# Kernel optimization log

Measured on AMD Instinct MI355X. Metric: run time of the kernel, lower is better.

Reference implementation:

```python
import jax, jax.numpy as jnp
import numpy as np
from jax import lax

WIN = 7
K1 = 0.01
K2 = 0.03


def _box(t, w):
    # 'valid' box filter: uniform WINxWIN window, matches F.conv2d(t, w)
    return lax.conv_general_dilated(
        t, w, window_strides=(1, 1), padding='VALID',
        dimension_numbers=('NCHW', 'OIHW', 'NCHW'))


def setup_inputs() -> dict:
    key = jax.random.key(0)
    kx, ky = jax.random.split(key)
    X = jax.random.uniform(kx, (256, 1, 320, 320), dtype=jnp.float32)
    Y = jax.random.uniform(ky, (256, 1, 320, 320), dtype=jnp.float32)
    return {"X": X, "Y": Y}


def reference(X, Y):
    NP = WIN * WIN
    cov_norm = NP / (NP - 1)  # unbiased covariance correction
    w = jnp.ones((1, 1, WIN, WIN), X.dtype) / NP

    # per-sample dynamic range of the reference image Y -> [B,1,1,1]
    data_range = jnp.max(Y, axis=(1, 2, 3), keepdims=True)
    C1 = (K1 * data_range) ** 2
    C2 = (K2 * data_range) ** 2

    ux = _box(X, w)
    uy = _box(Y, w)
    uxx = _box(X * X, w)
    uyy = _box(Y * Y, w)
    uxy = _box(X * Y, w)

    vx = cov_norm * (uxx - ux * ux)
    vy = cov_norm * (uyy - uy * uy)
    vxy = cov_norm * (uxy - ux * uy)

    A1 = 2 * ux * uy + C1
    A2 = 2 * vxy + C2
    B1 = ux * ux + uy * uy + C1
    B2 = vx + vy + C2

    S = (A1 * A2) / (B1 * B2)
    S = jnp.mean(S)          # reduced=True
    return 1.0 - S           # as_loss=True
```

## Files before the change

kernel.cpp:

```cpp
#include <hip/hip_runtime.h>

#define BATCH 256
#define IMH 320
#define IMW 320
#define OUTD 314
#define NCH 9
#define NSTRIP 3
#define RCH 36
#define ITERS 42

__global__ __launch_bounds__(256) void k_max(const float* __restrict__ Y,
                                             unsigned* __restrict__ dr) {
    int bid = blockIdx.x;
    int b = bid >> 2, part = bid & 3;
    const float4* p = (const float4*)(Y + (size_t)b * (IMH * IMW) + part * (IMH * IMW / 4));
    float m = 0.f;
    for (int i = threadIdx.x; i < (IMH * IMW / 16); i += 256) {
        float4 v = p[i];
        m = fmaxf(m, fmaxf(fmaxf(v.x, v.y), fmaxf(v.z, v.w)));
    }
    for (int off = 32; off; off >>= 1) m = fmaxf(m, __shfl_down(m, off, 64));
    __shared__ float sm[4];
    int lane = threadIdx.x & 63, wv = threadIdx.x >> 6;
    if (lane == 0) sm[wv] = m;
    __syncthreads();
    if (threadIdx.x == 0) {
        m = fmaxf(fmaxf(sm[0], sm[1]), fmaxf(sm[2], sm[3]));
        atomicMax(dr + b, __float_as_uint(m));
    }
}

__device__ __forceinline__ float ssim_px(float hx, float hy, float hp, float hxy,
                                         float C1, float C2) {
    const float inv = 1.f / 49.f;
    const float cn  = 49.f / 48.f;
    float ux  = hx  * inv, uy = hy * inv;
    float upp = hp  * inv;
    float uxy = hxy * inv;
    float ux2 = ux * ux, uy2 = uy * uy, uxuy = ux * uy;
    float B2 = cn * (upp - ux2 - uy2) + C2;
    float A2 = 2.f * cn * (uxy - uxuy) + C2;
    float A1 = 2.f * uxuy + C1;
    float B1 = ux2 + uy2 + C1;
    return (A1 * A2) * __builtin_amdgcn_rcpf(B1 * B2);
}

__device__ __forceinline__ float bperm(int addr, float v) {
    return __int_as_float(__builtin_amdgcn_ds_bpermute(addr, __float_as_int(v)));
}

template<bool FULL>
__device__ __forceinline__ float strip_loop(const float2* __restrict__ Xp,
                                            const float2* __restrict__ Yp,
                                            int r0, int nout,
                                            int a1, int a2, int a3,
                                            bool valid, float C1, float C2) {
    float2 rx[7], ry[7];
    #pragma unroll
    for (int k = 0; k < 7; ++k) { rx[k] = make_float2(0.f, 0.f); ry[k] = make_float2(0.f, 0.f); }
    float2 sx  = make_float2(0.f, 0.f), sy  = make_float2(0.f, 0.f);
    float2 sp  = make_float2(0.f, 0.f), sxy = make_float2(0.f, 0.f);
    float part = 0.f;

    #define HQ(q, h0, h1) {                                                    \
        float s2_ = q.x + q.y;                                                 \
        float b1_ = bperm(a1, s2_);                                            \
        float b2_ = bperm(a2, s2_);                                            \
        float b3_ = bperm(a3, s2_);                                            \
        float y3_ = bperm(a3, q.y);                                            \
        float S8_ = (s2_ + b1_) + (b2_ + b3_);                                 \
        h0 = S8_ - y3_;  h1 = S8_ - q.x; }

    #define VBODY(K, I7) {                                                     \
        const int i = (I7) + (K);                                              \
        const int r = r0 + i;                                                  \
        float2 xn = make_float2(0.f, 0.f), yn = make_float2(0.f, 0.f);         \
        if (FULL || r < IMH) { xn = Xp[r * (IMW/2)]; yn = Yp[r * (IMW/2)]; }   \
        const float2 ox = rx[K], oy = ry[K];                                   \
        sx.x  += xn.x - ox.x;              sx.y  += xn.y - ox.y;               \
        sy.x  += yn.x - oy.x;              sy.y  += yn.y - oy.y;               \
        sp.x  += (xn.x*xn.x + yn.x*yn.x) - (ox.x*ox.x + oy.x*oy.x);            \
        sp.y  += (xn.y*xn.y + yn.y*yn.y) - (ox.y*ox.y + oy.y*oy.y);            \
        sxy.x += xn.x*yn.x - ox.x*oy.x;    sxy.y += xn.y*yn.y - ox.y*oy.y;     \
        rx[K] = xn; ry[K] = yn;                                                \
        if (i >= 6 && (FULL || (i - 6) < nout)) {                              \
            float hx0,hx1,hy0,hy1,hp0,hp1,hq0,hq1;                             \
            HQ(sx,  hx0, hx1)                                                  \
            HQ(sy,  hy0, hy1)                                                  \
            HQ(sp,  hp0, hp1)                                                  \
            HQ(sxy, hq0, hq1)                                                  \
            float s0 = ssim_px(hx0, hy0, hp0, hq0, C1, C2);                    \
            float s1 = ssim_px(hx1, hy1, hp1, hq1, C1, C2);                    \
            part += valid ? (s0 + s1) : 0.f;                                   \
        }                                                                      \
    }

    for (int i7 = 0; i7 < ITERS; i7 += 7) {
        VBODY(0, i7) VBODY(1, i7) VBODY(2, i7) VBODY(3, i7)
        VBODY(4, i7) VBODY(5, i7) VBODY(6, i7)
    }
    #undef VBODY
    #undef HQ
    return part;
}

__global__ __launch_bounds__(64) void k_ssim(const float* __restrict__ X,
                                             const float* __restrict__ Y,
                                             const unsigned* __restrict__ dr,
                                             double* __restrict__ acc) {
    const int idx = blockIdx.x;
    const int b   = idx / (NCH * NSTRIP);
    const int rem = idx - b * (NCH * NSTRIP);
    const int rc  = rem / NSTRIP;
    const int s   = rem - rc * NSTRIP;
    const int l   = threadIdx.x;
    const int r0  = rc * RCH;
    const int nout = min(RCH, OUTD - r0);

    const int in_base = (s == 0) ? 0 : (s == 1 ? 122 : 192);
    const int lane_lo = (s == 2) ? 26 : 0;
    const bool valid  = (l >= lane_lo) && (l <= 60);

    const float2* Xp = (const float2*)(X + (size_t)b * (IMH * IMW)) + (in_base >> 1) + l;
    const float2* Yp = (const float2*)(Y + (size_t)b * (IMH * IMW)) + (in_base >> 1) + l;

    const int a1 = ((l + 1) & 63) << 2;
    const int a2 = ((l + 2) & 63) << 2;
    const int a3 = ((l + 3) & 63) << 2;

    const float drv = __uint_as_float(dr[b]);
    const float c1s = 0.01f * drv, c2s = 0.03f * drv;
    const float C1 = c1s * c1s, C2 = c2s * c2s;

    float part;
    if (r0 + ITERS <= IMH) {
        part = strip_loop<true >(Xp, Yp, r0, nout, a1, a2, a3, valid, C1, C2);
    } else {
        part = strip_loop<false>(Xp, Yp, r0, nout, a1, a2, a3, valid, C1, C2);
    }

    for (int off = 32; off; off >>= 1) part += __shfl_down(part, off, 64);
    if (l == 0) atomicAdd(acc, (double)part);
}

__global__ void k_final(const double* __restrict__ acc, float* __restrict__ out) {
    const double cnt = (double)BATCH * (double)OUTD * (double)OUTD;
    out[0] = (float)(1.0 - acc[0] / cnt);
}

extern "C" void kernel_launch(void* const* d_in, const int* in_sizes, int n_in,
                              void* d_out, int out_size, void* d_ws, size_t ws_size,
                              hipStream_t stream) {
    const float* X = (const float*)d_in[0];
    const float* Y = (const float*)d_in[1];
    float* out = (float*)d_out;

    unsigned* dr = (unsigned*)d_ws;
    double* acc  = (double*)((char*)d_ws + 1024);

    hipMemsetAsync(d_ws, 0, 2048, stream);
    k_max <<<BATCH * 4, 256, 0, stream>>>(Y, dr);
    k_ssim<<<BATCH * NCH * NSTRIP, 64, 0, stream>>>(X, Y, dr, acc);
    k_final<<<1, 1, 0, stream>>>(acc, out);
}
```

Measured before the change: 322.7 us.

## Use DPP row shifts for horizontal sums and 16-lane row groups

The horizontal 7-wide window sum now uses DPP row_shl lane shifts instead of ds_bpermute. Because DPP shifts stay inside a 16-lane row, the work is split into groups of 16 lanes, each covering 13 output pairs with overlap. A block is now 256 threads spanning the full image width instead of three 64-lane strips. The block reduces through shared memory before a single atomic. This removes LDS-crossbar permutes and cuts redundant halo loads across strips, at the cost of overlapping loads between the 16-lane groups.

```diff
diff --git a/kernel.cpp b/kernel.cpp
--- a/kernel.cpp
+++ b/kernel.cpp
@@ -5,7 +5,6 @@
 #define IMW 320
 #define OUTD 314
 #define NCH 9
-#define NSTRIP 3
 #define RCH 36
 #define ITERS 42
 
@@ -45,15 +44,16 @@
     return (A1 * A2) * __builtin_amdgcn_rcpf(B1 * B2);
 }
 
-__device__ __forceinline__ float bperm(int addr, float v) {
-    return __int_as_float(__builtin_amdgcn_ds_bpermute(addr, __float_as_int(v)));
+template<int K>
+__device__ __forceinline__ float dppshl(float v) {
+    return __int_as_float(__builtin_amdgcn_update_dpp(
+        0, __float_as_int(v), 0x100 + K, 0xF, 0xF, true));
 }
 
 template<bool FULL>
 __device__ __forceinline__ float strip_loop(const float2* __restrict__ Xp,
                                             const float2* __restrict__ Yp,
                                             int r0, int nout,
-                                            int a1, int a2, int a3,
                                             bool valid, float C1, float C2) {
     float2 rx[7], ry[7];
     #pragma unroll
@@ -64,12 +64,10 @@
 
     #define HQ(q, h0, h1) {                                                    \
         float s2_ = q.x + q.y;                                                 \
-        float b1_ = bperm(a1, s2_);                                            \
-        float b2_ = bperm(a2, s2_);                                            \
-        float b3_ = bperm(a3, s2_);                                            \
-        float y3_ = bperm(a3, q.y);                                            \
-        float S8_ = (s2_ + b1_) + (b2_ + b3_);                                 \
-        h0 = S8_ - y3_;  h1 = S8_ - q.x; }
+        float t1_ = s2_ + dppshl<1>(s2_);                                      \
+        float S4_ = t1_ + dppshl<2>(t1_);                                      \
+        float y3_ = dppshl<3>(q.y);                                            \
+        h0 = S4_ - y3_;  h1 = S4_ - q.x; }
 
     #define VBODY(K, I7) {                                                     \
         const int i = (I7) + (K);                                              \
@@ -104,29 +102,23 @@
     return part;
 }
 
-__global__ __launch_bounds__(64) void k_ssim(const float* __restrict__ X,
-                                             const float* __restrict__ Y,
-                                             const unsigned* __restrict__ dr,
-                                             double* __restrict__ acc) {
+__global__ __launch_bounds__(256) void k_ssim(const float* __restrict__ X,
+                                              const float* __restrict__ Y,
+                                              const unsigned* __restrict__ dr,
+                                              double* __restrict__ acc) {
     const int idx = blockIdx.x;
-    const int b   = idx / (NCH * NSTRIP);
-    const int rem = idx - b * (NCH * NSTRIP);
-    const int rc  = rem / NSTRIP;
-    const int s   = rem - rc * NSTRIP;
-    const int l   = threadIdx.x;
+    const int b   = idx / NCH;
+    const int rc  = idx - b * NCH;
+    const int t   = threadIdx.x;
+    const int g   = t >> 4, j = t & 15;
     const int r0  = rc * RCH;
     const int nout = min(RCH, OUTD - r0);
 
-    const int in_base = (s == 0) ? 0 : (s == 1 ? 122 : 192);
-    const int lane_lo = (s == 2) ? 26 : 0;
-    const bool valid  = (l >= lane_lo) && (l <= 60);
+    const bool valid = (g < 12 && j <= 12) || (g == 12 && j == 0);
+    const int fidx = min(13 * g + j, (IMW / 2) - 1);
 
-    const float2* Xp = (const float2*)(X + (size_t)b * (IMH * IMW)) + (in_base >> 1) + l;
-    const float2* Yp = (const float2*)(Y + (size_t)b * (IMH * IMW)) + (in_base >> 1) + l;
-
-    const int a1 = ((l + 1) & 63) << 2;
-    const int a2 = ((l + 2) & 63) << 2;
-    const int a3 = ((l + 3) & 63) << 2;
+    const float2* Xp = (const float2*)(X + (size_t)b * (IMH * IMW)) + fidx;
+    const float2* Yp = (const float2*)(Y + (size_t)b * (IMH * IMW)) + fidx;
 
     const float drv = __uint_as_float(dr[b]);
     const float c1s = 0.01f * drv, c2s = 0.03f * drv;
@@ -134,13 +126,17 @@
 
     float part;
     if (r0 + ITERS <= IMH) {
-        part = strip_loop<true >(Xp, Yp, r0, nout, a1, a2, a3, valid, C1, C2);
+        part = strip_loop<true >(Xp, Yp, r0, nout, valid, C1, C2);
     } else {
-        part = strip_loop<false>(Xp, Yp, r0, nout, a1, a2, a3, valid, C1, C2);
+        part = strip_loop<false>(Xp, Yp, r0, nout, valid, C1, C2);
     }
 
     for (int off = 32; off; off >>= 1) part += __shfl_down(part, off, 64);
-    if (l == 0) atomicAdd(acc, (double)part);
+    __shared__ float ps[4];
+    const int lane = t & 63, wv = t >> 6;
+    if (lane == 0) ps[wv] = part;
+    __syncthreads();
+    if (t == 0) atomicAdd(acc, (double)((ps[0] + ps[1]) + (ps[2] + ps[3])));
 }
 
 __global__ void k_final(const double* __restrict__ acc, float* __restrict__ out) {
@@ -160,6 +156,6 @@
 
     hipMemsetAsync(d_ws, 0, 2048, stream);
     k_max <<<BATCH * 4, 256, 0, stream>>>(Y, dr);
-    k_ssim<<<BATCH * NCH * NSTRIP, 64, 0, stream>>>(X, Y, dr, acc);
+    k_ssim<<<BATCH * NCH, 256, 0, stream>>>(X, Y, dr, acc);
     k_final<<<1, 1, 0, stream>>>(acc, out);
 }
```

After: 268.5 us. -16.8%, faster.
